# Performance work log

Measured on AMD Instinct MI355X. Metric: run time of the kernel, lower is better.

## Reference

```python
import jax, jax.numpy as jnp
import numpy as np

DT = 0.01
V_REST = 0.0


def setup_inputs() -> dict:
    key = jax.random.key(0)
    ks = jax.random.split(key, 9)
    S, N, T = 64, 128, 1000
    w = jax.random.normal(ks[0], (N, N), dtype=jnp.float32) / jnp.sqrt(jnp.float32(N))
    ic = jax.random.uniform(ks[1], (N,), dtype=jnp.float32)
    v0 = jax.random.uniform(ks[2], (S, N), dtype=jnp.float32)
    i0 = jax.random.uniform(ks[3], (S, N), dtype=jnp.float32)
    # spike-clock state starts at minus an Exponential(1) draw; event fires when it hits 0
    u0 = jax.random.uniform(ks[4], (S, N), dtype=jnp.float32, minval=1e-6, maxval=1.0)
    s0 = jnp.log(u0)
    mu = jax.random.uniform(ks[5], (2,), dtype=jnp.float32, minval=0.5, maxval=1.0)
    sg = jax.random.normal(ks[6], (2, 2), dtype=jnp.float32)
    sigma = 0.1 * jnp.dot(sg, sg.T)  # PSD diffusion matrix as in __init__
    noise = jax.random.normal(ks[7], (T, S, N, 2), dtype=jnp.float32)
    ue = jax.random.uniform(ks[8], (T, S, N), dtype=jnp.float32, minval=1e-6, maxval=1.0)
    exp_draws = -jnp.log(ue)
    return {"w": w, "ic": ic, "v0": v0, "i0": i0, "s0": s0,
            "mu": mu, "sigma": sigma, "noise": noise, "exp_draws": exp_draws}


def reference(w, ic, v0, i0, s0, mu, sigma, noise, exp_draws):
    """Euler-Maruyama integration of the spiking-neuron jump-SDE.

    Per neuron state y = (v, i, s):
      dv = mu1*(i + ic - v) dt + (sigma dW)_0
      di = -mu2*i dt        + (sigma dW)_1
      ds = intensity_fn(v) dt   (intensity_fn = softplus)
    Spike event when s crosses 0 (cond_fn = y[:, 2]):
      v -> v_rest, postsynaptic currents i += spikes @ w, s -> -Exp(1) redraw.
    Returns ys of shape (samples, neurons, times, 3).
    """
    mu1, mu2 = mu[0], mu[1]
    dW = noise * jnp.sqrt(jnp.asarray(DT, noise.dtype))  # [T,S,N,2]

    def step(carry, xs):
        v, i, s = carry
        dw, edraw = xs
        # drift
        dv = mu1 * (i + ic - v)
        di = -mu2 * i
        ds = jax.nn.softplus(v)  # intensity_fn
        # diffusion on (v,i) channels: sigma @ dW per neuron
        nvi = jnp.einsum('snk,jk->snj', dw, sigma)  # [S,N,2]
        v = v + DT * dv + nvi[..., 0]
        i = i + DT * di + nvi[..., 1]
        s = s + DT * ds
        spike = s >= 0.0  # event detection (cond_fn hits zero)
        spk = spike.astype(v.dtype)
        i = i + spk @ w                    # network coupling jump
        v = jnp.where(spike, V_REST, v)    # membrane reset
        s = jnp.where(spike, -edraw, s)    # redraw exponential spike clock
        return (v, i, s), jnp.stack([v, i, s], axis=-1)  # [S,N,3]

    (_, _, _), ys = jax.lax.scan(step, (v0, i0, s0), (dW, exp_draws))
    # ys: [T,S,N,3] -> [S,N,T,3] (samples, neurons, times, 3)
    return jnp.transpose(ys, (1, 2, 0, 3))
```

## Files before the change

### kernel.cpp

```cpp
#include <hip/hip_runtime.h>
#include <cmath>

#define NS 64
#define NN 128
#define NT 1000
#define CH 8
#define WROWS 130
#define WL_DW (WROWS * NN)
#define OBUF_DW (2 * CH * 3 * NN)
#define LDS_BYTES ((WL_DW + OBUF_DW) * 4 + 32)

__device__ __forceinline__ float softplus_np(float x) {
    float r = fmaxf(x, 0.0f) + log1pf(expf(-fabsf(x)));
    return (x == 0.0f) ? 0.693147180559945309f : r;
}

__device__ __forceinline__ void sync_lds() {
    __builtin_amdgcn_sched_barrier(0);
    asm volatile("s_waitcnt lgkmcnt(0)" ::: "memory");
    __builtin_amdgcn_s_barrier();
    __builtin_amdgcn_sched_barrier(0);
}

__global__ __launch_bounds__(192) void snn_scan_kernel(
    const float* __restrict__ w,
    const float* __restrict__ ic,
    const float* __restrict__ v0,
    const float* __restrict__ i0,
    const float* __restrict__ s0,
    const float* __restrict__ mu,
    const float* __restrict__ sigma,
    const float* __restrict__ noise,
    const float* __restrict__ exp_draws,
    float* __restrict__ out)
{
    #pragma clang fp contract(off)
    extern __shared__ float smem[];
    float* wl   = smem;
    float* obuf = smem + WL_DW;
    unsigned long long* mslot =
        (unsigned long long*)(smem + WL_DW + OBUF_DW);

    const int samp = blockIdx.x;
    const int tid  = threadIdx.x;
    const int wid  = tid >> 6;
    const int l    = tid & 63;
    const int n    = (wid << 6) | l;

    if (tid < 128) {
        const float4* src = (const float4*)w;
        float4* dst = (float4*)wl;
        #pragma unroll
        for (int it = 0; it < 32; ++it)
            dst[it * 128 + tid] = src[it * 128 + tid];
        ((float2*)(wl + NN * NN))[tid] = make_float2(0.0f, 0.0f);
    }

    const float SQDT  = sqrtf(0.01f);
    const float DTf   = 0.01f;
    const float LOGE2 = 0.693147180559945309f;

    float* outb = out + (size_t)samp * NN * NT * 3;

    float mu1 = 0.f, negmu2 = 0.f, g00 = 0.f, g01 = 0.f, g10 = 0.f, g11 = 0.f;
    float icn = 0.f, v_ = 0.f, i_ = 0.f, s_ = 0.f, sp = 0.f;
    float2 nb0 = {}, nb1 = {}, nb2 = {}, nb3 = {}, nb4 = {}, nb5 = {}, nb6 = {}, nb7 = {};
    float  eb0 = 0, eb1 = 0, eb2 = 0, eb3 = 0, eb4 = 0, eb5 = 0, eb6 = 0, eb7 = 0;

    const float* nzb = noise + (size_t)samp * (NN * 2) + n * 2;
    const float* edb = exp_draws + (size_t)samp * NN + n;

    if (wid < 2) {
        __builtin_amdgcn_s_setprio(1);
        mu1 = mu[0]; negmu2 = -mu[1];
        g00 = sigma[0]; g01 = sigma[1]; g10 = sigma[2]; g11 = sigma[3];
        icn = ic[n];
        v_ = v0[samp * NN + n];
        i_ = i0[samp * NN + n];
        s_ = s0[samp * NN + n];
        sp = softplus_np(v_);
        nb0 = *(const float2*)(nzb + 0ull * (NS * NN * 2)); eb0 = edb[0ull * (NS * NN)];
        nb1 = *(const float2*)(nzb + 1ull * (NS * NN * 2)); eb1 = edb[1ull * (NS * NN)];
        nb2 = *(const float2*)(nzb + 2ull * (NS * NN * 2)); eb2 = edb[2ull * (NS * NN)];
        nb3 = *(const float2*)(nzb + 3ull * (NS * NN * 2)); eb3 = edb[3ull * (NS * NN)];
        nb4 = *(const float2*)(nzb + 4ull * (NS * NN * 2)); eb4 = edb[4ull * (NS * NN)];
        nb5 = *(const float2*)(nzb + 5ull * (NS * NN * 2)); eb5 = edb[5ull * (NS * NN)];
        nb6 = *(const float2*)(nzb + 6ull * (NS * NN * 2)); eb6 = edb[6ull * (NS * NN)];
        nb7 = *(const float2*)(nzb + 7ull * (NS * NN * 2)); eb7 = edb[7ull * (NS * NN)];
    }
    sync_lds();

    if (wid < 2) {
        int cur = 0;
        float* ob = obuf + n;

        auto STEP = [&](int k, int blk, float2& nb, float& eb) {
            #pragma clang fp contract(off)
            const int t = blk * CH + k;
            s_ = s_ + DTf * sp;
            const bool kk = (s_ >= 0.0f);
            const unsigned long long mym = __ballot(kk);
            if (l == 0) mslot[(k & 1) * 2 + wid] = mym;
            sync_lds();
            const float2 nz = nb;
            const float  ed = eb;
            const int tp = (t + 8) < NT ? (t + 8) : NT - 1;
            nb = *(const float2*)(nzb + (size_t)tp * (NS * NN * 2));
            eb = edb[(size_t)tp * (NS * NN)];

            const float dw0 = nz.x * SQDT, dw1 = nz.y * SQDT;
            const float nv = (dw0 * g00) + (dw1 * g01);
            const float ni = (dw0 * g10) + (dw1 * g11);
            const float tt = (i_ + icn) - v_;
            const float vt = (v_ + DTf * (mu1 * tt)) + nv;
            const float it = (i_ + DTf * (negmu2 * i_)) + ni;
            const float spv = softplus_np(vt);

            unsigned long long m0 = mslot[(k & 1) * 2 + 0];
            unsigned long long m1 = mslot[(k & 1) * 2 + 1];

            float a = 0.0f;
            if (m0 | m1) {
                auto ext1 = [&]() -> int {
                    const bool u0 = (m0 != 0);
                    const unsigned long long m = u0 ? m0 : m1;
                    const int b = m ? (int)__builtin_ctzll(m) : 99;
                    const int r = (b == 99) ? 128 : ((u0 ? 0 : 64) + b);
                    const unsigned long long m0n = m0 & (m0 - 1);
                    const unsigned long long m1n = m1 & (m1 - 1);
                    m0 = u0 ? m0n : m0;
                    m1 = u0 ? m1 : m1n;
                    return r;
                };
                const int r1 = ext1(); const int r2 = ext1();
                const int r3 = ext1(); const int r4 = ext1();
                const float q1 = wl[r1 * NN + n];
                const float q2 = wl[r2 * NN + n];
                const float q3 = wl[r3 * NN + n];
                const float q4 = wl[r4 * NN + n];
                a = q1;  a += q2;  a += q3;  a += q4;
                #pragma clang loop unroll(disable)
                while (m0 | m1) {
                    const int r = ext1();
                    a += wl[r * NN + n];
                }
            }
            i_ = it + a;

            v_ = kk ? 0.0f : vt;
            s_ = kk ? -ed : s_;
            sp = kk ? LOGE2 : spv;

            float* row = ob + (cur * CH * 3 + k * 3) * NN;
            row[0 * NN] = v_;
            row[1 * NN] = i_;
            row[2 * NN] = s_;
        };

        #pragma clang loop unroll(disable)
        for (int blk = 0; blk < NT / CH; ++blk) {
            STEP(0, blk, nb0, eb0);
            STEP(1, blk, nb1, eb1);
            STEP(2, blk, nb2, eb2);
            STEP(3, blk, nb3, eb3);
            STEP(4, blk, nb4, eb4);
            STEP(5, blk, nb5, eb5);
            STEP(6, blk, nb6, eb6);
            STEP(7, blk, nb7, eb7);
            cur ^= 1;
        }
    } else {
        auto flush3 = [&](int b, int tb0, int kk) {
            const float* ob2 = obuf + b * (CH * 3 * NN);
            #pragma unroll
            for (int j = 3 * kk; j < 3 * kk + 3; ++j) {
                const int f = j * 64 + l;
                const int nn2 = f / 12;
                const int da = 2 * (f - nn2 * 12);
                const float x = ob2[(da    ) * NN + nn2];
                const float y = ob2[(da + 1) * NN + nn2];
                *(float2*)(outb + (size_t)nn2 * (NT * 3) + (size_t)tb0 * 3 + da) =
                    make_float2(x, y);
            }
        };
        int cur = 0;
        #pragma clang loop unroll(disable)
        for (int blk = 0; blk < NT / CH; ++blk) {
            #pragma clang loop unroll(disable)
            for (int k = 0; k < CH; ++k) {
                sync_lds();
                if (blk > 0) flush3(cur ^ 1, (blk - 1) * CH, k);
            }
            cur ^= 1;
        }
    }

    sync_lds();

    if (wid == 2) {
        const float* ob2 = obuf + 0 * (CH * 3 * NN);
        #pragma unroll
        for (int j = 0; j < 24; ++j) {
            const int f = j * 64 + l;
            const int nn2 = f / 12;
            const int da = 2 * (f - nn2 * 12);
            const float x = ob2[(da    ) * NN + nn2];
            const float y = ob2[(da + 1) * NN + nn2];
            *(float2*)(outb + (size_t)nn2 * (NT * 3) + (size_t)(NT - CH) * 3 + da) =
                make_float2(x, y);
        }
    }
}

extern "C" void kernel_launch(void* const* d_in, const int* in_sizes, int n_in,
                              void* d_out, int out_size, void* d_ws, size_t ws_size,
                              hipStream_t stream) {
    const float* w         = (const float*)d_in[0];
    const float* ic        = (const float*)d_in[1];
    const float* v0        = (const float*)d_in[2];
    const float* i0        = (const float*)d_in[3];
    const float* s0        = (const float*)d_in[4];
    const float* mu        = (const float*)d_in[5];
    const float* sigma     = (const float*)d_in[6];
    const float* noise     = (const float*)d_in[7];
    const float* exp_draws = (const float*)d_in[8];
    float* out = (float*)d_out;

    (void)hipFuncSetAttribute((const void*)snn_scan_kernel,
                              hipFuncAttributeMaxDynamicSharedMemorySize,
                              LDS_BYTES);

    snn_scan_kernel<<<dim3(NS), dim3(192), LDS_BYTES, stream>>>(
        w, ic, v0, i0, s0, mu, sigma, noise, exp_draws, out);
}
```

Measured before the change: 575.4 us.

## Software-pipeline spike mask exchange one step ahead and pad output LDS buffer

Restructures the per-timestep loop so each step computes the next step's spike clock and publishes its ballot mask before the barrier. The following step then reads the masks at the start and issues the first four weight-row gathers before the drift math. This takes the barrier and mask read off the critical path between event detection and the coupling sum. It also pads the output staging rows to 129 floats to cut LDS bank conflicts in the transpose flush, and drops the scheduling barriers around the sync so the compiler can schedule more freely. The four weight gathers now run every step, hitting a zero padding row when fewer neurons spike.

```diff
diff --git a/kernel.cpp b/kernel.cpp
--- a/kernel.cpp
+++ b/kernel.cpp
@@ -5,9 +5,11 @@
 #define NN 128
 #define NT 1000
 #define CH 8
+#define NNP 129
 #define WROWS 130
 #define WL_DW (WROWS * NN)
-#define OBUF_DW (2 * CH * 3 * NN)
+#define OB_HALF (3 * CH * NNP)
+#define OBUF_DW (2 * OB_HALF)
 #define LDS_BYTES ((WL_DW + OBUF_DW) * 4 + 32)
 
 __device__ __forceinline__ float softplus_np(float x) {
@@ -16,10 +18,9 @@
 }
 
 __device__ __forceinline__ void sync_lds() {
-    __builtin_amdgcn_sched_barrier(0);
     asm volatile("s_waitcnt lgkmcnt(0)" ::: "memory");
     __builtin_amdgcn_s_barrier();
-    __builtin_amdgcn_sched_barrier(0);
+    asm volatile("" ::: "memory");
 }
 
 __global__ __launch_bounds__(192) void snn_scan_kernel(
@@ -63,7 +64,9 @@
     float* outb = out + (size_t)samp * NN * NT * 3;
 
     float mu1 = 0.f, negmu2 = 0.f, g00 = 0.f, g01 = 0.f, g10 = 0.f, g11 = 0.f;
-    float icn = 0.f, v_ = 0.f, i_ = 0.f, s_ = 0.f, sp = 0.f;
+    float icn = 0.f, v_ = 0.f, i_ = 0.f, s_ = 0.f;
+    bool  kk = false;
+    unsigned long long m0r = 0ull, m1r = 0ull;
     float2 nb0 = {}, nb1 = {}, nb2 = {}, nb3 = {}, nb4 = {}, nb5 = {}, nb6 = {}, nb7 = {};
     float  eb0 = 0, eb1 = 0, eb2 = 0, eb3 = 0, eb4 = 0, eb5 = 0, eb6 = 0, eb7 = 0;
 
@@ -78,7 +81,11 @@
         v_ = v0[samp * NN + n];
         i_ = i0[samp * NN + n];
         s_ = s0[samp * NN + n];
-        sp = softplus_np(v_);
+        const float sp0 = softplus_np(v_);
+        s_ = s_ + DTf * sp0;
+        kk = (s_ >= 0.0f);
+        const unsigned long long mym = __ballot(kk);
+        if (l == 0) mslot[0 * 2 + wid] = mym;
         nb0 = *(const float2*)(nzb + 0ull * (NS * NN * 2)); eb0 = edb[0ull * (NS * NN)];
         nb1 = *(const float2*)(nzb + 1ull * (NS * NN * 2)); eb1 = edb[1ull * (NS * NN)];
         nb2 = *(const float2*)(nzb + 2ull * (NS * NN * 2)); eb2 = edb[2ull * (NS * NN)];
@@ -91,17 +98,31 @@
     sync_lds();
 
     if (wid < 2) {
-        int cur = 0;
-        float* ob = obuf + n;
+        m0r = mslot[0];
+        m1r = mslot[1];
 
         auto STEP = [&](int k, int blk, float2& nb, float& eb) {
             #pragma clang fp contract(off)
             const int t = blk * CH + k;
-            s_ = s_ + DTf * sp;
-            const bool kk = (s_ >= 0.0f);
-            const unsigned long long mym = __ballot(kk);
-            if (l == 0) mslot[(k & 1) * 2 + wid] = mym;
-            sync_lds();
+            unsigned long long m0 = m0r, m1 = m1r;
+            auto ext1 = [&]() -> int {
+                const bool u0 = (m0 != 0);
+                const unsigned long long m = u0 ? m0 : m1;
+                const int b = m ? (int)__builtin_ctzll(m) : 99;
+                const int r = (b == 99) ? 128 : ((u0 ? 0 : 64) + b);
+                const unsigned long long m0n = m0 & (m0 - 1);
+                const unsigned long long m1n = m1 & (m1 - 1);
+                m0 = u0 ? m0n : m0;
+                m1 = u0 ? m1 : m1n;
+                return r;
+            };
+            const int r1 = ext1(); const int r2 = ext1();
+            const int r3 = ext1(); const int r4 = ext1();
+            const float q1 = wl[r1 * NN + n];
+            const float q2 = wl[r2 * NN + n];
+            const float q3 = wl[r3 * NN + n];
+            const float q4 = wl[r4 * NN + n];
+
             const float2 nz = nb;
             const float  ed = eb;
             const int tp = (t + 8) < NT ? (t + 8) : NT - 1;
@@ -116,45 +137,37 @@
             const float it = (i_ + DTf * (negmu2 * i_)) + ni;
             const float spv = softplus_np(vt);
 
-            unsigned long long m0 = mslot[(k & 1) * 2 + 0];
-            unsigned long long m1 = mslot[(k & 1) * 2 + 1];
-
-            float a = 0.0f;
+            float a = q1;
+            a += q2;  a += q3;  a += q4;
             if (m0 | m1) {
-                auto ext1 = [&]() -> int {
-                    const bool u0 = (m0 != 0);
-                    const unsigned long long m = u0 ? m0 : m1;
-                    const int b = m ? (int)__builtin_ctzll(m) : 99;
-                    const int r = (b == 99) ? 128 : ((u0 ? 0 : 64) + b);
-                    const unsigned long long m0n = m0 & (m0 - 1);
-                    const unsigned long long m1n = m1 & (m1 - 1);
-                    m0 = u0 ? m0n : m0;
-                    m1 = u0 ? m1 : m1n;
-                    return r;
-                };
-                const int r1 = ext1(); const int r2 = ext1();
-                const int r3 = ext1(); const int r4 = ext1();
-                const float q1 = wl[r1 * NN + n];
-                const float q2 = wl[r2 * NN + n];
-                const float q3 = wl[r3 * NN + n];
-                const float q4 = wl[r4 * NN + n];
-                a = q1;  a += q2;  a += q3;  a += q4;
                 #pragma clang loop unroll(disable)
-                while (m0 | m1) {
+                do {
                     const int r = ext1();
                     a += wl[r * NN + n];
-                }
+                } while (m0 | m1);
             }
             i_ = it + a;
 
-            v_ = kk ? 0.0f : vt;
-            s_ = kk ? -ed : s_;
-            sp = kk ? LOGE2 : spv;
-
-            float* row = ob + (cur * CH * 3 + k * 3) * NN;
-            row[0 * NN] = v_;
-            row[1 * NN] = i_;
-            row[2 * NN] = s_;
+            const float vn = kk ? 0.0f : vt;
+            const float sn = kk ? -ed : s_;
+            const float sp = kk ? LOGE2 : spv;
+
+            s_ = sn + DTf * sp;
+            const bool kk2 = (s_ >= 0.0f);
+            const unsigned long long mym = __ballot(kk2);
+            const int par1 = (t + 1) & 1;
+            if (l == 0) mslot[par1 * 2 + wid] = mym;
+            v_ = vn;
+
+            sync_lds();
+
+            m0r = mslot[par1 * 2 + 0];
+            m1r = mslot[par1 * 2 + 1];
+            kk = kk2;
+            float* row = obuf + (blk & 1) * OB_HALF + (k * 3) * NNP + n;
+            row[0 * NNP] = vn;
+            row[1 * NNP] = i_;
+            row[2 * NNP] = sn;
         };
 
         #pragma clang loop unroll(disable)
@@ -167,45 +180,41 @@
             STEP(5, blk, nb5, eb5);
             STEP(6, blk, nb6, eb6);
             STEP(7, blk, nb7, eb7);
-            cur ^= 1;
         }
     } else {
-        auto flush3 = [&](int b, int tb0, int kk) {
-            const float* ob2 = obuf + b * (CH * 3 * NN);
+        auto flush3 = [&](int h, int tb0, int kk2) {
+            const float* ob2 = obuf + h * OB_HALF;
             #pragma unroll
-            for (int j = 3 * kk; j < 3 * kk + 3; ++j) {
+            for (int j = 3 * kk2; j < 3 * kk2 + 3; ++j) {
                 const int f = j * 64 + l;
                 const int nn2 = f / 12;
                 const int da = 2 * (f - nn2 * 12);
-                const float x = ob2[(da    ) * NN + nn2];
-                const float y = ob2[(da + 1) * NN + nn2];
+                const float x = ob2[(da    ) * NNP + nn2];
+                const float y = ob2[(da + 1) * NNP + nn2];
                 *(float2*)(outb + (size_t)nn2 * (NT * 3) + (size_t)tb0 * 3 + da) =
                     make_float2(x, y);
             }
         };
-        int cur = 0;
         #pragma clang loop unroll(disable)
         for (int blk = 0; blk < NT / CH; ++blk) {
             #pragma clang loop unroll(disable)
             for (int k = 0; k < CH; ++k) {
                 sync_lds();
-                if (blk > 0) flush3(cur ^ 1, (blk - 1) * CH, k);
+                if (blk > 0) flush3((blk - 1) & 1, (blk - 1) * CH, k);
             }
-            cur ^= 1;
         }
     }
 
     sync_lds();
-
     if (wid == 2) {
-        const float* ob2 = obuf + 0 * (CH * 3 * NN);
+        const float* ob2 = obuf + ((NT / CH - 1) & 1) * OB_HALF;
         #pragma unroll
         for (int j = 0; j < 24; ++j) {
             const int f = j * 64 + l;
             const int nn2 = f / 12;
             const int da = 2 * (f - nn2 * 12);
-            const float x = ob2[(da    ) * NN + nn2];
-            const float y = ob2[(da + 1) * NN + nn2];
+            const float x = ob2[(da    ) * NNP + nn2];
+            const float y = ob2[(da + 1) * NNP + nn2];
             *(float2*)(outb + (size_t)nn2 * (NT * 3) + (size_t)(NT - CH) * 3 + da) =
                 make_float2(x, y);
         }
```

Result: slower. 630.9 us (+9.6%).
